# Kernel optimization log

Measured on AMD Instinct MI355X. Metric: run time of the kernel, lower is better.

Reference implementation:

```python
import jax, jax.numpy as jnp
import numpy as np

PI = np.pi
EPS_A = 1e-4


def _frft_1d(x, a):
    """Chirp-z shear FRFT along the last axis. x: complex (..., N), a: scalar order."""
    a = jnp.clip(a, EPS_A, 2.0 - EPS_A)
    N = x.shape[-1]
    x = jnp.fft.ifftshift(x, axes=-1)
    alpha = a * PI / 2.0
    tan_a2 = jnp.tan(a * PI / 4.0)
    sin_a = jnp.sin(alpha)
    n = (jnp.arange(N, dtype=jnp.float32) - (N // 2))  # [-N/2, N/2)
    c1 = jnp.exp(-1j * PI * (n ** 2) * tan_a2 / N)      # chirp (depends on a)
    c2 = jnp.exp(-1j * PI * (n ** 2) / (N * sin_a))     # kernel chirp
    y = jnp.fft.ifft(jnp.fft.fft(x * c1, axis=-1) * c2, axis=-1)
    y = y * c1 / jnp.sqrt(jnp.abs(sin_a) + 1e-12)
    return jnp.fft.fftshift(y, axes=-1)


def _frft2d(x, ax, ay):
    # width pass (last axis) with ay, then height pass with ax -- same math as the
    # per-row / per-column torch loops, fully batched.
    y = _frft_1d(x, ay)                                   # over W
    y = jnp.swapaxes(_frft_1d(jnp.swapaxes(y, -1, -2), ax), -1, -2)  # over H
    return y


def setup_inputs() -> dict:
    key = jax.random.key(0)
    kx, = jax.random.split(key, 1)
    B, C, H, W = 4, 32, 256, 256
    x = jax.random.normal(kx, (B, C, H, W), dtype=jnp.float32)
    alpha = jnp.float32(0.5)
    # 1x1 conv weight (C, 2C): module init = copy of magnitude channels
    w = jnp.zeros((C, 2 * C), dtype=jnp.float32)
    w = w.at[jnp.arange(C), jnp.arange(C)].set(1.0)
    return {"x": x, "alpha": alpha, "w": w}


def reference(x, alpha, w):
    Xc = x.astype(jnp.complex64)
    Y = _frft2d(Xc, alpha, alpha)                        # (B, C, H, W) complex
    out = jnp.concatenate([jnp.abs(Y), jnp.angle(Y) / PI], axis=1)  # (B, 2C, H, W)
    out = jnp.einsum('oc,bchw->bohw', w, out)            # 1x1 conv, no bias
    return out.astype(x.dtype)
```

## Files before the change

kernel.cpp:

```cpp
#include <hip/hip_runtime.h>
#include <math.h>

#define B_N 4
#define C_N 32
#define H_N 256
#define W_N 256
#define PI_D 3.14159265358979323846
#define LSQ 257
#define LDW 260
#define LTS 36

typedef _Float16 half8 __attribute__((ext_vector_type(8)));
typedef float f32x4 __attribute__((ext_vector_type(4)));

__device__ __forceinline__ float2 cmul(float2 a, float2 b) {
    return make_float2(a.x * b.x - a.y * b.y, a.x * b.y + a.y * b.x);
}
__device__ __forceinline__ float2 f2add(float2 a, float2 b) {
    return make_float2(a.x + b.x, a.y + b.y);
}
__device__ __forceinline__ float2 f2sub(float2 a, float2 b) {
    return make_float2(a.x - b.x, a.y - b.y);
}

__device__ __forceinline__ void make_tables(int tid, const float* __restrict__ alpha_p,
                                            float2* c1l, float2* c2l, float2* twl,
                                            float* sscl) {
    if (tid < 256) {
        int j = tid;
        float a = fminf(fmaxf(alpha_p[0], 1e-4f), 2.0f - 1e-4f);
        float tan_a2 = tanf(a * (float)(PI_D / 4.0));
        float sin_a  = sinf(a * (float)(PI_D / 2.0));
        float n = (float)(j - 128);
        float n2f = n * n;
        float sn, cs;

        float u1 = n2f * tan_a2 * (1.0f / 256.0f);
        u1 -= 2.0f * floorf(u1 * 0.5f);
        __sincosf(-(float)PI_D * u1, &sn, &cs);
        c1l[j] = make_float2(cs, sn);

        float u2 = n2f / (256.0f * sin_a);
        u2 -= 2.0f * floorf(u2 * 0.5f);
        __sincosf(-(float)PI_D * u2, &sn, &cs);
        c2l[j] = make_float2(cs, sn);

        int k1 = j >> 4, t = j & 15;
        __sincosf(-(float)(2.0 * PI_D / 256.0) * (float)(t * k1), &sn, &cs);
        twl[j] = make_float2(cs, sn);

        if (j == 0) *sscl = 1.0f / sqrtf(sin_a + 1e-12f);
    }
}

template <bool INV>
__device__ __forceinline__ void fft16(float2* v) {
    const float C1 = 0.9238795325112867f, S1 = 0.3826834323650898f;
    const float C2 = 0.7071067811865476f;
    const float2 tw1 = make_float2(C1, INV ? S1 : -S1);
    const float2 tw2 = make_float2(C2, INV ? C2 : -C2);
    const float2 tw3 = make_float2(S1, INV ? C1 : -C1);
    const float2 tw4 = make_float2(0.0f, INV ? 1.0f : -1.0f);
    const float2 tw6 = make_float2(-C2, INV ? C2 : -C2);
    const float2 tw9 = make_float2(-C1, INV ? -S1 : S1);
    float2 u[16];
    #pragma unroll
    for (int n2 = 0; n2 < 4; ++n2) {
        float2 e0 = v[n2], e1 = v[4 + n2], e2 = v[8 + n2], e3 = v[12 + n2];
        float2 t0 = f2add(e0, e2), t1 = f2sub(e0, e2);
        float2 t2 = f2add(e1, e3), t3 = f2sub(e1, e3);
        float2 A0 = f2add(t0, t2);
        float2 A2 = f2sub(t0, t2);
        float2 A1, A3;
        if (!INV) { A1 = make_float2(t1.x + t3.y, t1.y - t3.x);
                    A3 = make_float2(t1.x - t3.y, t1.y + t3.x); }
        else      { A1 = make_float2(t1.x - t3.y, t1.y + t3.x);
                    A3 = make_float2(t1.x + t3.y, t1.y - t3.x); }
        u[n2] = A0;
        if (n2 == 0) { u[4 + n2] = A1;            u[8 + n2] = A2;            u[12 + n2] = A3; }
        if (n2 == 1) { u[4 + n2] = cmul(A1, tw1); u[8 + n2] = cmul(A2, tw2); u[12 + n2] = cmul(A3, tw3); }
        if (n2 == 2) { u[4 + n2] = cmul(A1, tw2); u[8 + n2] = cmul(A2, tw4); u[12 + n2] = cmul(A3, tw6); }
        if (n2 == 3) { u[4 + n2] = cmul(A1, tw3); u[8 + n2] = cmul(A2, tw6); u[12 + n2] = cmul(A3, tw9); }
    }
    #pragma unroll
    for (int k1 = 0; k1 < 4; ++k1) {
        float2 e0 = u[4 * k1], e1 = u[4 * k1 + 1], e2 = u[4 * k1 + 2], e3 = u[4 * k1 + 3];
        float2 t0 = f2add(e0, e2), t1 = f2sub(e0, e2);
        float2 t2 = f2add(e1, e3), t3 = f2sub(e1, e3);
        v[4 * k1 + 0] = f2add(t0, t2);
        v[4 * k1 + 2] = f2sub(t0, t2);
        if (!INV) { v[4 * k1 + 1] = make_float2(t1.x + t3.y, t1.y - t3.x);
                    v[4 * k1 + 3] = make_float2(t1.x - t3.y, t1.y + t3.x); }
        else      { v[4 * k1 + 1] = make_float2(t1.x - t3.y, t1.y + t3.x);
                    v[4 * k1 + 3] = make_float2(t1.x + t3.y, t1.y - t3.x); }
    }
}
#define REG(k) (4 * ((k) & 3) + ((k) >> 2))

template <bool WL>
__device__ __forceinline__ void core_sync() {
    if (WL) __builtin_amdgcn_wave_barrier();
    else    __syncthreads();
}

template <bool WL>
__device__ __forceinline__ void frft_core16(float2* v, float2* __restrict__ sp,
                                            int t,
                                            const float2* __restrict__ c2l,
                                            const float2* __restrict__ twl) {
    fft16<false>(v);
    float2 w[16];
    #pragma unroll
    for (int k1 = 0; k1 < 16; ++k1)
        w[k1] = cmul(v[REG(k1)], twl[16 * k1 + t]);
    #pragma unroll
    for (int k1 = 0; k1 < 16; ++k1)
        sp[16 * k1 + (t ^ k1)] = w[k1];
    core_sync<WL>();
    #pragma unroll
    for (int n2 = 0; n2 < 16; ++n2)
        v[n2] = sp[16 * t + (n2 ^ t)];
    fft16<false>(v);
    #pragma unroll
    for (int k2 = 0; k2 < 16; ++k2)
        w[k2] = cmul(v[REG(k2)], c2l[t + 16 * k2]);
    fft16<true>(w);
    core_sync<WL>();
    #pragma unroll
    for (int m2 = 0; m2 < 16; ++m2) {
        float2 tw = twl[16 * m2 + t];
        tw.y = -tw.y;
        sp[16 * m2 + (t ^ m2)] = cmul(w[REG(m2)], tw);
    }
    core_sync<WL>();
    #pragma unroll
    for (int k1 = 0; k1 < 16; ++k1)
        v[k1] = sp[16 * t + (k1 ^ t)];
    fft16<true>(v);
}

__global__ __launch_bounds__(512, 4) void frft_cols_real(
        const float* __restrict__ x,
        const float* __restrict__ alpha_p,
        float2* __restrict__ Y) {
    __shared__ float2 s[32 * LSQ];
    __shared__ float2 c1l[256], c2l[256], twl[256];
    __shared__ float sscl;
    int tid = threadIdx.x;

    int blk = blockIdx.x;
    int w0 = (blk & 7) << 5;
    long long bc = blk >> 3;
    const float* xb = x + (bc << 16) + w0;

    float4 xv[4];
    #pragma unroll
    for (int p = 0; p < 4; ++p) {
        int idx = tid + (p << 9);
        int row = idx >> 3, c4 = idx & 7;
        xv[p] = *(const float4*)(xb + row * W_N + (c4 << 2));
    }

    make_tables(tid, alpha_p, c1l, c2l, twl, &sscl);

    float* fs = (float*)s;
    #pragma unroll
    for (int p = 0; p < 4; ++p) {
        int idx = tid + (p << 9);
        int row = idx >> 3, c4 = idx & 7;
        *(float4*)&fs[row * LTS + (c4 << 2)] = xv[p];
    }
    __syncthreads();

    int seq = tid & 31, t = tid >> 5;
    float xs[16];
    #pragma unroll
    for (int n1 = 0; n1 < 16; ++n1)
        xs[n1] = fs[(16 * (n1 ^ 8) + t) * LTS + seq];
    float scl_v = sscl;
    __syncthreads();

    float2 v[16];
    #pragma unroll
    for (int n1 = 0; n1 < 16; ++n1) {
        float2 c = c1l[16 * n1 + t];
        v[n1] = make_float2(xs[n1] * c.x, xs[n1] * c.y);
    }

    frft_core16<false>(v, s + seq * LSQ, t, c2l, twl);

    float sc = scl_v * (1.0f / 256.0f);
    float2* Yb = Y + (bc << 16) + w0 + seq;
    #pragma unroll
    for (int m1 = 0; m1 < 16; ++m1) {
        float2 o = cmul(v[REG(m1)], c1l[16 * m1 + t]);
        Yb[(16 * (m1 ^ 8) + t) * W_N] = make_float2(o.x * sc, o.y * sc);
    }
}

__device__ __forceinline__ float fast_atan2(float y, float x) {
    float ax = fabsf(x), ay = fabsf(y);
    float mx = fmaxf(ax, ay), mn = fminf(ax, ay);
    float z = mn * __builtin_amdgcn_rcpf(fmaxf(mx, 1e-37f));
    float z2 = z * z;
    float p = fmaf(z2, -0.01172120f, 0.05265332f);
    p = fmaf(z2, p, -0.11643287f);
    p = fmaf(z2, p, 0.19354346f);
    p = fmaf(z2, p, -0.33262347f);
    p = fmaf(z2, p, 0.99997726f);
    p = p * z;
    float r = (ay > ax) ? (1.5707963f - p) : p;
    r = (x < 0.0f) ? (3.14159265f - r) : r;
    return copysignf(r, y);
}

__global__ __launch_bounds__(512, 4) void frft_rows_conv(
        const float2* __restrict__ Y,
        const float* __restrict__ alpha_p,
        const float* __restrict__ wmat, float* __restrict__ out) {
    __shared__ float2 s[32 * LSQ];
    __shared__ float2 c1l[256], c2l[256], twl[256];
    __shared__ float sscl;
    int tid = threadIdx.x;
    int t = tid & 15, ch = tid >> 4;

    int b = blockIdx.x >> 8, h = blockIdx.x & 255;
    const float2* xr = Y + (((long long)(b * C_N + ch)) << 16) + (h << 8);

    float2 v[16];
    #pragma unroll
    for (int n1 = 0; n1 < 16; ++n1)
        v[n1] = xr[16 * (n1 ^ 8) + t];

    make_tables(tid, alpha_p, c1l, c2l, twl, &sscl);
    __syncthreads();

    #pragma unroll
    for (int n1 = 0; n1 < 16; ++n1)
        v[n1] = cmul(v[n1], c1l[16 * n1 + t]);

    float2* sp = s + ch * LSQ;
    frft_core16<true>(v, sp, t, c2l, twl);

    float sc = sscl * (1.0f / 256.0f);
    #pragma unroll
    for (int m1 = 0; m1 < 16; ++m1) {
        float2 o = cmul(v[REG(m1)], c1l[16 * m1 + t]);
        float mg = sc * sqrtf(fmaf(o.x, o.x, o.y * o.y));
        float an = fast_atan2(o.y, o.x) * 0.31830988618f;
        sp[16 * (m1 ^ 8) + t] = make_float2(mg, an);
    }
    __syncthreads();

    int lane = tid & 63, wv = tid >> 6;
    int q = lane >> 4, l15 = lane & 15;

    half8 bf[2][2];
    #pragma unroll
    for (int nt = 0; nt < 2; ++nt)
        #pragma unroll
        for (int kt = 0; kt < 2; ++kt) {
            const float* wp = wmat + (nt * 16 + l15) * 64 + kt * 32 + q * 8;
            float4 wa = *(const float4*)wp;
            float4 wb = *(const float4*)(wp + 4);
            bf[nt][kt][0] = (_Float16)wa.x; bf[nt][kt][1] = (_Float16)wa.y;
            bf[nt][kt][2] = (_Float16)wa.z; bf[nt][kt][3] = (_Float16)wa.w;
            bf[nt][kt][4] = (_Float16)wb.x; bf[nt][kt][5] = (_Float16)wb.y;
            bf[nt][kt][6] = (_Float16)wb.z; bf[nt][kt][7] = (_Float16)wb.w;
        }

    f32x4 acc[2][2];
    #pragma unroll
    for (int i = 0; i < 2; ++i)
        #pragma unroll
        for (int j = 0; j < 2; ++j)
            acc[i][j] = (f32x4){0.0f, 0.0f, 0.0f, 0.0f};

    #pragma unroll
    for (int mt2 = 0; mt2 < 2; ++mt2) {
        int mt = wv * 2 + mt2;
        int w = mt * 16 + l15;
        half8 am, aa;
        #pragma unroll
        for (int j = 0; j < 8; ++j) {
            float2 fv = s[(q * 8 + j) * LSQ + w];
            am[j] = (_Float16)fv.x;
            aa[j] = (_Float16)fv.y;
        }
        #pragma unroll
        for (int nt = 0; nt < 2; ++nt) {
            acc[mt2][nt] = __builtin_amdgcn_mfma_f32_16x16x32_f16(am, bf[nt][0], acc[mt2][nt], 0, 0, 0);
            acc[mt2][nt] = __builtin_amdgcn_mfma_f32_16x16x32_f16(aa, bf[nt][1], acc[mt2][nt], 0, 0, 0);
        }
    }
    __syncthreads();

    float* Ob = (float*)s;
    #pragma unroll
    for (int mt2 = 0; mt2 < 2; ++mt2) {
        int mt = wv * 2 + mt2;
        #pragma unroll
        for (int nt = 0; nt < 2; ++nt) {
            int o = nt * 16 + l15;
            *(f32x4*)&Ob[o * LDW + mt * 16 + q * 4] = acc[mt2][nt];
        }
    }
    __syncthreads();

    int o2 = tid >> 4, i16 = tid & 15;
    float* ob = out + (((long long)(b * C_N + o2)) << 16) + (h << 8);
    #pragma unroll
    for (int p = 0; p < 4; ++p) {
        int w4 = i16 * 4 + (p << 6);
        f32x4 val = *(f32x4*)&Ob[o2 * LDW + w4];
        *(f32x4*)(ob + w4) = val;
    }
}

extern "C" void kernel_launch(void* const* d_in, const int* in_sizes, int n_in,
                              void* d_out, int out_size, void* d_ws, size_t ws_size,
                              hipStream_t stream) {
    const float* x     = (const float*)d_in[0];
    const float* alpha = (const float*)d_in[1];
    const float* wmat  = (const float*)d_in[2];
    float* out = (float*)d_out;

    float2* Y = (float2*)d_ws;

    frft_cols_real<<<B_N * C_N * (W_N / 32), 512, 0, stream>>>(x, alpha, Y);

    frft_rows_conv<<<B_N * H_N, 512, 0, stream>>>(Y, alpha, wmat, out);
}
```

Before: 132.3 us.

## Process two column tiles per block, pad LDS transpose, write conv output directly

The column FRFT kernel now handles 64 columns per block in two halves. It prefetches the second half's global loads while the first half is computed, which halves the grid and amortises the chirp/twiddle table setup. The LDS transpose inside the FFT core switches from XOR swizzling to a padded row stride, so each row can be read back with vectorised 16-byte loads. The row/conv kernel drops the LDS staging of its MFMA outputs and stores accumulators straight to global memory. That removes two barriers but makes the global writes less coalesced.

```diff
diff --git a/kernel.cpp b/kernel.cpp
--- a/kernel.cpp
+++ b/kernel.cpp
@@ -6,8 +6,8 @@
 #define H_N 256
 #define W_N 256
 #define PI_D 3.14159265358979323846
-#define LSQ 257
-#define LDW 260
+#define CR  18
+#define LSQ 286
 #define LTS 36
 
 typedef _Float16 half8 __attribute__((ext_vector_type(8)));
@@ -97,6 +97,15 @@
 }
 #define REG(k) (4 * ((k) & 3) + ((k) >> 2))
 
+__device__ __forceinline__ void lds_read_row16(const float2* __restrict__ rp, float2* v) {
+    #pragma unroll
+    for (int c = 0; c < 8; ++c) {
+        f32x4 r = *(const f32x4*)(rp + 2 * c);
+        v[2 * c]     = make_float2(r.x, r.y);
+        v[2 * c + 1] = make_float2(r.z, r.w);
+    }
+}
+
 template <bool WL>
 __device__ __forceinline__ void core_sync() {
     if (WL) __builtin_amdgcn_wave_barrier();
@@ -115,11 +124,9 @@
         w[k1] = cmul(v[REG(k1)], twl[16 * k1 + t]);
     #pragma unroll
     for (int k1 = 0; k1 < 16; ++k1)
-        sp[16 * k1 + (t ^ k1)] = w[k1];
+        sp[CR * k1 + t] = w[k1];
     core_sync<WL>();
-    #pragma unroll
-    for (int n2 = 0; n2 < 16; ++n2)
-        v[n2] = sp[16 * t + (n2 ^ t)];
+    lds_read_row16(sp + CR * t, v);
     fft16<false>(v);
     #pragma unroll
     for (int k2 = 0; k2 < 16; ++k2)
@@ -130,12 +137,10 @@
     for (int m2 = 0; m2 < 16; ++m2) {
         float2 tw = twl[16 * m2 + t];
         tw.y = -tw.y;
-        sp[16 * m2 + (t ^ m2)] = cmul(w[REG(m2)], tw);
+        sp[CR * m2 + t] = cmul(w[REG(m2)], tw);
     }
     core_sync<WL>();
-    #pragma unroll
-    for (int k1 = 0; k1 < 16; ++k1)
-        v[k1] = sp[16 * t + (k1 ^ t)];
+    lds_read_row16(sp + CR * t, v);
     fft16<true>(v);
 }
 
@@ -149,8 +154,8 @@
     int tid = threadIdx.x;
 
     int blk = blockIdx.x;
-    int w0 = (blk & 7) << 5;
-    long long bc = blk >> 3;
+    int w0 = (blk & 3) << 6;
+    long long bc = blk >> 2;
     const float* xb = x + (bc << 16) + w0;
 
     float4 xv[4];
@@ -163,38 +168,53 @@
 
     make_tables(tid, alpha_p, c1l, c2l, twl, &sscl);
 
+    int seq = tid & 31, t = tid >> 5;
+    float2* sp = s + seq * LSQ;
     float* fs = (float*)s;
-    #pragma unroll
-    for (int p = 0; p < 4; ++p) {
-        int idx = tid + (p << 9);
-        int row = idx >> 3, c4 = idx & 7;
-        *(float4*)&fs[row * LTS + (c4 << 2)] = xv[p];
-    }
-    __syncthreads();
-
-    int seq = tid & 31, t = tid >> 5;
-    float xs[16];
-    #pragma unroll
-    for (int n1 = 0; n1 < 16; ++n1)
-        xs[n1] = fs[(16 * (n1 ^ 8) + t) * LTS + seq];
-    float scl_v = sscl;
-    __syncthreads();
-
-    float2 v[16];
-    #pragma unroll
-    for (int n1 = 0; n1 < 16; ++n1) {
-        float2 c = c1l[16 * n1 + t];
-        v[n1] = make_float2(xs[n1] * c.x, xs[n1] * c.y);
-    }
-
-    frft_core16<false>(v, s + seq * LSQ, t, c2l, twl);
-
-    float sc = scl_v * (1.0f / 256.0f);
-    float2* Yb = Y + (bc << 16) + w0 + seq;
-    #pragma unroll
-    for (int m1 = 0; m1 < 16; ++m1) {
-        float2 o = cmul(v[REG(m1)], c1l[16 * m1 + t]);
-        Yb[(16 * (m1 ^ 8) + t) * W_N] = make_float2(o.x * sc, o.y * sc);
+
+    #pragma unroll
+    for (int half = 0; half < 2; ++half) {
+        #pragma unroll
+        for (int p = 0; p < 4; ++p) {
+            int idx = tid + (p << 9);
+            int row = idx >> 3, c4 = idx & 7;
+            *(float4*)&fs[row * LTS + (c4 << 2)] = xv[p];
+        }
+        __syncthreads();
+
+        float xs[16];
+        #pragma unroll
+        for (int n1 = 0; n1 < 16; ++n1)
+            xs[n1] = fs[(16 * (n1 ^ 8) + t) * LTS + seq];
+        float scl_v = sscl;
+
+        if (half == 0) {
+            #pragma unroll
+            for (int p = 0; p < 4; ++p) {
+                int idx = tid + (p << 9);
+                int row = idx >> 3, c4 = idx & 7;
+                xv[p] = *(const float4*)(xb + 32 + row * W_N + (c4 << 2));
+            }
+        }
+        __syncthreads();
+
+        float2 v[16];
+        #pragma unroll
+        for (int n1 = 0; n1 < 16; ++n1) {
+            float2 c = c1l[16 * n1 + t];
+            v[n1] = make_float2(xs[n1] * c.x, xs[n1] * c.y);
+        }
+
+        frft_core16<false>(v, sp, t, c2l, twl);
+
+        float sc = scl_v * (1.0f / 256.0f);
+        float2* Yb = Y + (bc << 16) + w0 + (half << 5) + seq;
+        #pragma unroll
+        for (int m1 = 0; m1 < 16; ++m1) {
+            float2 o = cmul(v[REG(m1)], c1l[16 * m1 + t]);
+            Yb[(16 * (m1 ^ 8) + t) * W_N] = make_float2(o.x * sc, o.y * sc);
+        }
+        if (half == 0) __syncthreads();
     }
 }
 
@@ -293,27 +313,16 @@
             acc[mt2][nt] = __builtin_amdgcn_mfma_f32_16x16x32_f16(aa, bf[nt][1], acc[mt2][nt], 0, 0, 0);
         }
     }
-    __syncthreads();
-
-    float* Ob = (float*)s;
+
     #pragma unroll
     for (int mt2 = 0; mt2 < 2; ++mt2) {
         int mt = wv * 2 + mt2;
         #pragma unroll
         for (int nt = 0; nt < 2; ++nt) {
             int o = nt * 16 + l15;
-            *(f32x4*)&Ob[o * LDW + mt * 16 + q * 4] = acc[mt2][nt];
-        }
-    }
-    __syncthreads();
-
-    int o2 = tid >> 4, i16 = tid & 15;
-    float* ob = out + (((long long)(b * C_N + o2)) << 16) + (h << 8);
-    #pragma unroll
-    for (int p = 0; p < 4; ++p) {
-        int w4 = i16 * 4 + (p << 6);
-        f32x4 val = *(f32x4*)&Ob[o2 * LDW + w4];
-        *(f32x4*)(ob + w4) = val;
+            float* op = out + (((long long)(b * C_N + o)) << 16) + (h << 8) + mt * 16 + q * 4;
+            *(f32x4*)op = acc[mt2][nt];
+        }
     }
 }
 
@@ -327,7 +336,7 @@
 
     float2* Y = (float2*)d_ws;
 
-    frft_cols_real<<<B_N * C_N * (W_N / 32), 512, 0, stream>>>(x, alpha, Y);
+    frft_cols_real<<<B_N * C_N * (W_N / 64), 512, 0, stream>>>(x, alpha, Y);
 
     frft_rows_conv<<<B_N * H_N, 512, 0, stream>>>(Y, alpha, wmat, out);
 }
```

Result: slower. 137.1 us (+3.6%).

## Shrink LDS footprint with wave-local half-tile transposes and packed fp16 features

Applied to the files above, without the earlier changes.

The in-FFT transposes now use a small per-sequence LDS region with two half passes and wave barriers, instead of a full 256-element scratch per sequence. The column kernel remaps threads so each 16-lane group owns one sequence, which removes block-wide syncs. The row kernel packs magnitude and angle into fp16 pairs in a channel-contiguous layout for vectorized MFMA operand loads, and writes conv results straight to global with nontemporal stores rather than staging them through LDS. Together with the smaller shared memory, occupancy hints rise from 4 to 6 blocks per CU, at the cost of more barriers and extra LDS passes per transpose.

```diff
diff --git a/kernel.cpp b/kernel.cpp
--- a/kernel.cpp
+++ b/kernel.cpp
@@ -6,12 +6,15 @@
 #define H_N 256
 #define W_N 256
 #define PI_D 3.14159265358979323846
-#define LSQ 257
-#define LDW 260
-#define LTS 36
+#define CR   18
+#define SEQS 146
+#define LTS  36
+#define FTS  36
 
 typedef _Float16 half8 __attribute__((ext_vector_type(8)));
 typedef float f32x4 __attribute__((ext_vector_type(4)));
+
+union H2U { unsigned int u; struct { _Float16 lo, hi; } f; };
 
 __device__ __forceinline__ float2 cmul(float2 a, float2 b) {
     return make_float2(a.x * b.x - a.y * b.y, a.x * b.y + a.y * b.x);
@@ -97,13 +100,31 @@
 }
 #define REG(k) (4 * ((k) & 3) + ((k) >> 2))
 
-template <bool WL>
-__device__ __forceinline__ void core_sync() {
-    if (WL) __builtin_amdgcn_wave_barrier();
-    else    __syncthreads();
-}
-
-template <bool WL>
+__device__ __forceinline__ void lds_read_row16(const float2* __restrict__ rp, float2* v) {
+    #pragma unroll
+    for (int c = 0; c < 8; ++c) {
+        f32x4 r = *(const f32x4*)(rp + 2 * c);
+        v[2 * c]     = make_float2(r.x, r.y);
+        v[2 * c + 1] = make_float2(r.z, r.w);
+    }
+}
+
+__device__ __forceinline__ void xpose16(const float2* a, float2* o,
+                                        float2* __restrict__ sp, int t) {
+    bool lo = (t & 8) == 0;
+    float2* rp = sp + CR * (t & 7);
+    #pragma unroll
+    for (int r = 0; r < 8; ++r) sp[CR * r + t] = a[r];
+    __builtin_amdgcn_wave_barrier();
+    if (lo) lds_read_row16(rp, o);
+    __builtin_amdgcn_wave_barrier();
+    #pragma unroll
+    for (int r = 0; r < 8; ++r) sp[CR * r + t] = a[8 + r];
+    __builtin_amdgcn_wave_barrier();
+    if (!lo) lds_read_row16(rp, o);
+    __builtin_amdgcn_wave_barrier();
+}
+
 __device__ __forceinline__ void frft_core16(float2* v, float2* __restrict__ sp,
                                             int t,
                                             const float2* __restrict__ c2l,
@@ -113,37 +134,29 @@
     #pragma unroll
     for (int k1 = 0; k1 < 16; ++k1)
         w[k1] = cmul(v[REG(k1)], twl[16 * k1 + t]);
-    #pragma unroll
-    for (int k1 = 0; k1 < 16; ++k1)
-        sp[16 * k1 + (t ^ k1)] = w[k1];
-    core_sync<WL>();
-    #pragma unroll
-    for (int n2 = 0; n2 < 16; ++n2)
-        v[n2] = sp[16 * t + (n2 ^ t)];
+    xpose16(w, v, sp, t);
     fft16<false>(v);
     #pragma unroll
     for (int k2 = 0; k2 < 16; ++k2)
         w[k2] = cmul(v[REG(k2)], c2l[t + 16 * k2]);
     fft16<true>(w);
-    core_sync<WL>();
     #pragma unroll
     for (int m2 = 0; m2 < 16; ++m2) {
         float2 tw = twl[16 * m2 + t];
         tw.y = -tw.y;
-        sp[16 * m2 + (t ^ m2)] = cmul(w[REG(m2)], tw);
-    }
-    core_sync<WL>();
-    #pragma unroll
-    for (int k1 = 0; k1 < 16; ++k1)
-        v[k1] = sp[16 * t + (k1 ^ t)];
-    fft16<true>(v);
-}
-
-__global__ __launch_bounds__(512, 4) void frft_cols_real(
+        v[m2] = cmul(w[REG(m2)], tw);
+    }
+    xpose16(v, w, sp, t);
+    fft16<true>(w);
+    #pragma unroll
+    for (int i = 0; i < 16; ++i) v[i] = w[i];
+}
+
+__global__ __launch_bounds__(512, 6) void frft_cols_real(
         const float* __restrict__ x,
         const float* __restrict__ alpha_p,
         float2* __restrict__ Y) {
-    __shared__ float2 s[32 * LSQ];
+    __shared__ float2 s[32 * SEQS];
     __shared__ float2 c1l[256], c2l[256], twl[256];
     __shared__ float sscl;
     int tid = threadIdx.x;
@@ -153,12 +166,12 @@
     long long bc = blk >> 3;
     const float* xb = x + (bc << 16) + w0;
 
-    float4 xv[4];
+    f32x4 xv[4];
     #pragma unroll
     for (int p = 0; p < 4; ++p) {
         int idx = tid + (p << 9);
         int row = idx >> 3, c4 = idx & 7;
-        xv[p] = *(const float4*)(xb + row * W_N + (c4 << 2));
+        xv[p] = __builtin_nontemporal_load((const f32x4*)(xb + row * W_N + (c4 << 2)));
     }
 
     make_tables(tid, alpha_p, c1l, c2l, twl, &sscl);
@@ -168,11 +181,11 @@
     for (int p = 0; p < 4; ++p) {
         int idx = tid + (p << 9);
         int row = idx >> 3, c4 = idx & 7;
-        *(float4*)&fs[row * LTS + (c4 << 2)] = xv[p];
-    }
-    __syncthreads();
-
-    int seq = tid & 31, t = tid >> 5;
+        *(f32x4*)&fs[row * LTS + (c4 << 2)] = xv[p];
+    }
+    __syncthreads();
+
+    int t = tid & 15, seq = tid >> 4;
     float xs[16];
     #pragma unroll
     for (int n1 = 0; n1 < 16; ++n1)
@@ -187,7 +200,7 @@
         v[n1] = make_float2(xs[n1] * c.x, xs[n1] * c.y);
     }
 
-    frft_core16<false>(v, s + seq * LSQ, t, c2l, twl);
+    frft_core16(v, s + seq * SEQS, t, c2l, twl);
 
     float sc = scl_v * (1.0f / 256.0f);
     float2* Yb = Y + (bc << 16) + w0 + seq;
@@ -214,11 +227,11 @@
     return copysignf(r, y);
 }
 
-__global__ __launch_bounds__(512, 4) void frft_rows_conv(
+__global__ __launch_bounds__(512, 6) void frft_rows_conv(
         const float2* __restrict__ Y,
         const float* __restrict__ alpha_p,
         const float* __restrict__ wmat, float* __restrict__ out) {
-    __shared__ float2 s[32 * LSQ];
+    __shared__ float2 s[32 * SEQS];
     __shared__ float2 c1l[256], c2l[256], twl[256];
     __shared__ float sscl;
     int tid = threadIdx.x;
@@ -239,17 +252,24 @@
     for (int n1 = 0; n1 < 16; ++n1)
         v[n1] = cmul(v[n1], c1l[16 * n1 + t]);
 
-    float2* sp = s + ch * LSQ;
-    frft_core16<true>(v, sp, t, c2l, twl);
+    frft_core16(v, s + ch * SEQS, t, c2l, twl);
 
     float sc = sscl * (1.0f / 256.0f);
+    unsigned int pk[16];
     #pragma unroll
     for (int m1 = 0; m1 < 16; ++m1) {
         float2 o = cmul(v[REG(m1)], c1l[16 * m1 + t]);
         float mg = sc * sqrtf(fmaf(o.x, o.x, o.y * o.y));
         float an = fast_atan2(o.y, o.x) * 0.31830988618f;
-        sp[16 * (m1 ^ 8) + t] = make_float2(mg, an);
-    }
+        H2U pu; pu.f.lo = (_Float16)mg; pu.f.hi = (_Float16)an;
+        pk[m1] = pu.u;
+    }
+    __syncthreads();
+
+    unsigned int* feat = (unsigned int*)s;
+    #pragma unroll
+    for (int m1 = 0; m1 < 16; ++m1)
+        feat[(16 * (m1 ^ 8) + t) * FTS + ch] = pk[m1];
     __syncthreads();
 
     int lane = tid & 63, wv = tid >> 6;
@@ -280,12 +300,16 @@
     for (int mt2 = 0; mt2 < 2; ++mt2) {
         int mt = wv * 2 + mt2;
         int w = mt * 16 + l15;
+        const uint4* fp = (const uint4*)(feat + w * FTS + q * 8);
+        uint4 ca = fp[0], cb = fp[1];
         half8 am, aa;
         #pragma unroll
         for (int j = 0; j < 8; ++j) {
-            float2 fv = s[(q * 8 + j) * LSQ + w];
-            am[j] = (_Float16)fv.x;
-            aa[j] = (_Float16)fv.y;
+            H2U pu;
+            pu.u = (j < 4) ? ((const unsigned int*)&ca)[j]
+                           : ((const unsigned int*)&cb)[j - 4];
+            am[j] = pu.f.lo;
+            aa[j] = pu.f.hi;
         }
         #pragma unroll
         for (int nt = 0; nt < 2; ++nt) {
@@ -293,27 +317,16 @@
             acc[mt2][nt] = __builtin_amdgcn_mfma_f32_16x16x32_f16(aa, bf[nt][1], acc[mt2][nt], 0, 0, 0);
         }
     }
-    __syncthreads();
-
-    float* Ob = (float*)s;
+
     #pragma unroll
     for (int mt2 = 0; mt2 < 2; ++mt2) {
         int mt = wv * 2 + mt2;
         #pragma unroll
         for (int nt = 0; nt < 2; ++nt) {
             int o = nt * 16 + l15;
-            *(f32x4*)&Ob[o * LDW + mt * 16 + q * 4] = acc[mt2][nt];
+            float* op = out + (((long long)(b * C_N + o)) << 16) + (h << 8) + mt * 16 + q * 4;
+            __builtin_nontemporal_store(acc[mt2][nt], (f32x4*)op);
         }
-    }
-    __syncthreads();
-
-    int o2 = tid >> 4, i16 = tid & 15;
-    float* ob = out + (((long long)(b * C_N + o2)) << 16) + (h << 8);
-    #pragma unroll
-    for (int p = 0; p < 4; ++p) {
-        int w4 = i16 * 4 + (p << 6);
-        f32x4 val = *(f32x4*)&Ob[o2 * LDW + w4];
-        *(f32x4*)(ob + w4) = val;
     }
 }
 
```

New measurement: 176.5 us. 33.4% more time.

## Store intermediate FRFT result in fp16 and transpose input tile via padded LDS

Applied to the files above, without the earlier changes.

The complex intermediate between the column and row passes is now packed as two fp16 values in one 32-bit word, which halves the global write and read traffic for the workspace. The input staging in LDS is transposed to a padded column-major layout, so each sequence reads contiguous addresses. The wave-local barriers in the row kernel become full block barriers. Together these aim to cut memory bandwidth, at the cost of fp16 precision loss in the intermediate and possibly more synchronisation overhead.

```diff
diff --git a/kernel.cpp b/kernel.cpp
--- a/kernel.cpp
+++ b/kernel.cpp
@@ -8,10 +8,11 @@
 #define PI_D 3.14159265358979323846
 #define LSQ 257
 #define LDW 260
-#define LTS 36
 
 typedef _Float16 half8 __attribute__((ext_vector_type(8)));
 typedef float f32x4 __attribute__((ext_vector_type(4)));
+
+union H2U { unsigned int u; struct { _Float16 lo, hi; } f; };
 
 __device__ __forceinline__ float2 cmul(float2 a, float2 b) {
     return make_float2(a.x * b.x - a.y * b.y, a.x * b.y + a.y * b.x);
@@ -97,13 +98,6 @@
 }
 #define REG(k) (4 * ((k) & 3) + ((k) >> 2))
 
-template <bool WL>
-__device__ __forceinline__ void core_sync() {
-    if (WL) __builtin_amdgcn_wave_barrier();
-    else    __syncthreads();
-}
-
-template <bool WL>
 __device__ __forceinline__ void frft_core16(float2* v, float2* __restrict__ sp,
                                             int t,
                                             const float2* __restrict__ c2l,
@@ -116,7 +110,7 @@
     #pragma unroll
     for (int k1 = 0; k1 < 16; ++k1)
         sp[16 * k1 + (t ^ k1)] = w[k1];
-    core_sync<WL>();
+    __syncthreads();
     #pragma unroll
     for (int n2 = 0; n2 < 16; ++n2)
         v[n2] = sp[16 * t + (n2 ^ t)];
@@ -125,14 +119,14 @@
     for (int k2 = 0; k2 < 16; ++k2)
         w[k2] = cmul(v[REG(k2)], c2l[t + 16 * k2]);
     fft16<true>(w);
-    core_sync<WL>();
+    __syncthreads();
     #pragma unroll
     for (int m2 = 0; m2 < 16; ++m2) {
         float2 tw = twl[16 * m2 + t];
         tw.y = -tw.y;
         sp[16 * m2 + (t ^ m2)] = cmul(w[REG(m2)], tw);
     }
-    core_sync<WL>();
+    __syncthreads();
     #pragma unroll
     for (int k1 = 0; k1 < 16; ++k1)
         v[k1] = sp[16 * t + (k1 ^ t)];
@@ -142,7 +136,7 @@
 __global__ __launch_bounds__(512, 4) void frft_cols_real(
         const float* __restrict__ x,
         const float* __restrict__ alpha_p,
-        float2* __restrict__ Y) {
+        unsigned int* __restrict__ Yh) {
     __shared__ float2 s[32 * LSQ];
     __shared__ float2 c1l[256], c2l[256], twl[256];
     __shared__ float sscl;
@@ -168,7 +162,10 @@
     for (int p = 0; p < 4; ++p) {
         int idx = tid + (p << 9);
         int row = idx >> 3, c4 = idx & 7;
-        *(float4*)&fs[row * LTS + (c4 << 2)] = xv[p];
+        fs[(4 * c4 + 0) * (2 * LSQ) + row] = xv[p].x;
+        fs[(4 * c4 + 1) * (2 * LSQ) + row] = xv[p].y;
+        fs[(4 * c4 + 2) * (2 * LSQ) + row] = xv[p].z;
+        fs[(4 * c4 + 3) * (2 * LSQ) + row] = xv[p].w;
     }
     __syncthreads();
 
@@ -176,7 +173,7 @@
     float xs[16];
     #pragma unroll
     for (int n1 = 0; n1 < 16; ++n1)
-        xs[n1] = fs[(16 * (n1 ^ 8) + t) * LTS + seq];
+        xs[n1] = fs[seq * (2 * LSQ) + 16 * (n1 ^ 8) + t];
     float scl_v = sscl;
     __syncthreads();
 
@@ -187,14 +184,17 @@
         v[n1] = make_float2(xs[n1] * c.x, xs[n1] * c.y);
     }
 
-    frft_core16<false>(v, s + seq * LSQ, t, c2l, twl);
+    frft_core16(v, s + seq * LSQ, t, c2l, twl);
 
     float sc = scl_v * (1.0f / 256.0f);
-    float2* Yb = Y + (bc << 16) + w0 + seq;
+    unsigned int* Yb = Yh + (bc << 16) + w0 + seq;
     #pragma unroll
     for (int m1 = 0; m1 < 16; ++m1) {
         float2 o = cmul(v[REG(m1)], c1l[16 * m1 + t]);
-        Yb[(16 * (m1 ^ 8) + t) * W_N] = make_float2(o.x * sc, o.y * sc);
+        H2U pu;
+        pu.f.lo = (_Float16)(o.x * sc);
+        pu.f.hi = (_Float16)(o.y * sc);
+        Yb[(16 * (m1 ^ 8) + t) * W_N] = pu.u;
     }
 }
 
@@ -215,7 +215,7 @@
 }
 
 __global__ __launch_bounds__(512, 4) void frft_rows_conv(
-        const float2* __restrict__ Y,
+        const unsigned int* __restrict__ Yh,
         const float* __restrict__ alpha_p,
         const float* __restrict__ wmat, float* __restrict__ out) {
     __shared__ float2 s[32 * LSQ];
@@ -225,12 +225,14 @@
     int t = tid & 15, ch = tid >> 4;
 
     int b = blockIdx.x >> 8, h = blockIdx.x & 255;
-    const float2* xr = Y + (((long long)(b * C_N + ch)) << 16) + (h << 8);
+    const unsigned int* xr = Yh + (((long long)(b * C_N + ch)) << 16) + (h << 8);
 
     float2 v[16];
     #pragma unroll
-    for (int n1 = 0; n1 < 16; ++n1)
-        v[n1] = xr[16 * (n1 ^ 8) + t];
+    for (int n1 = 0; n1 < 16; ++n1) {
+        H2U pu; pu.u = xr[16 * (n1 ^ 8) + t];
+        v[n1] = make_float2((float)pu.f.lo, (float)pu.f.hi);
+    }
 
     make_tables(tid, alpha_p, c1l, c2l, twl, &sscl);
     __syncthreads();
@@ -240,7 +242,7 @@
         v[n1] = cmul(v[n1], c1l[16 * n1 + t]);
 
     float2* sp = s + ch * LSQ;
-    frft_core16<true>(v, sp, t, c2l, twl);
+    frft_core16(v, sp, t, c2l, twl);
 
     float sc = sscl * (1.0f / 256.0f);
     #pragma unroll
@@ -325,9 +327,9 @@
     const float* wmat  = (const float*)d_in[2];
     float* out = (float*)d_out;
 
-    float2* Y = (float2*)d_ws;
-
-    frft_cols_real<<<B_N * C_N * (W_N / 32), 512, 0, stream>>>(x, alpha, Y);
-
-    frft_rows_conv<<<B_N * H_N, 512, 0, stream>>>(Y, alpha, wmat, out);
-}
+    unsigned int* Yh = (unsigned int*)d_ws;
+
+    frft_cols_real<<<B_N * C_N * (W_N / 32), 512, 0, stream>>>(x, alpha, Yh);
+
+    frft_rows_conv<<<B_N * H_N, 512, 0, stream>>>(Yh, alpha, wmat, out);
+}
```

Measured after the change: 125.6 us, median of 2. 1.05x faster.
